# Kernel optimization log

Hardware: AMD Instinct MI355X
Metric: run time of the kernel (lower is better)

Reference implementation:

```python
import jax, jax.numpy as jnp
import numpy as np

N = 100000   # nodes
E = 3200000  # directed edges
IN = 128     # in_channels
H = 16       # hidden_channels
OUT = 2      # out_channels
EPS = 1e-5   # BatchNorm eps


def setup_inputs() -> dict:
    key = jax.random.key(0)
    ks = jax.random.split(key, 16)
    x = jax.random.normal(ks[0], (N, IN), jnp.float32)
    edge_index = jax.random.randint(ks[1], (2, E), 0, N, jnp.int32)

    def lin(k, fan_in, fan_out):
        return jax.random.normal(k, (fan_in, fan_out), jnp.float32) / np.sqrt(fan_in)

    return {
        "x": x,
        "edge_index": edge_index,
        "W1": lin(ks[2], IN, H), "b1": jnp.zeros((H,), jnp.float32),
        "W2": lin(ks[3], H, H), "b2": jnp.zeros((H,), jnp.float32),
        "W3": lin(ks[4], H, H), "b3": jnp.zeros((H,), jnp.float32),
        "gamma1": jnp.ones((H,), jnp.float32), "beta1": jnp.zeros((H,), jnp.float32),
        "gamma2": jnp.ones((H,), jnp.float32), "beta2": jnp.zeros((H,), jnp.float32),
        "Wfc": lin(ks[5], H, OUT), "bfc": jnp.zeros((OUT,), jnp.float32),
    }


def reference(x, edge_index, W1, b1, W2, b2, W3, b3,
              gamma1, beta1, gamma2, beta2, Wfc, bfc):
    src, dst = edge_index[0], edge_index[1]
    # symmetric GCN normalization with self loops: deg includes +1 self loop
    deg = jax.ops.segment_sum(jnp.ones((E,), x.dtype), dst, num_segments=N) + 1.0
    dis = jax.lax.rsqrt(deg)                      # [N]
    norm = dis[src] * dis[dst]                    # [E]

    def gcn_conv(h, W, b):
        hw = h @ W                                # [N, F] dense transform
        msg = norm[:, None] * hw[src]             # gather + scale  [E, F]
        agg = jax.ops.segment_sum(msg, dst, num_segments=N)
        agg = agg + (dis * dis)[:, None] * hw     # self-loop contribution
        return agg + b

    def batch_norm(h, g, be):
        mu = h.mean(axis=0)
        var = h.var(axis=0)
        return (h - mu) * jax.lax.rsqrt(var + EPS) * g + be

    h = batch_norm(jax.nn.relu(gcn_conv(x, W1, b1)), gamma1, beta1)
    # dropout is identity in inference / deterministic reference
    h = batch_norm(jax.nn.relu(gcn_conv(h, W2, b2)), gamma2, beta2)
    h = gcn_conv(h, W3, b3)
    return jax.nn.log_softmax(h @ Wfc + bfc, axis=1)
```

## Files before the change

### kernel.cpp

```cpp
#include <hip/hip_runtime.h>
#include <hip/hip_fp16.h>

#define NN 100000
#define EE 3200000
#define INC 128
#define HC 16
#define BN_EPS 1e-5f

#define NPB 256
#define NBUCK ((NN + NPB - 1) / NPB)
#define CAP 9216
#define BINSZ ((size_t)NBUCK * CAP)
#define BTILE 4096
#define BGRID ((EE + BTILE - 1) / BTILE)
#define SB_CAP 12288
#define GGRID 2048

#define XSTR 132

__device__ __forceinline__ __half2 bits_to_h2(int v) { __half2 h; *(int*)&h = v; return h; }
__device__ __forceinline__ int h2_to_bits(__half2 h) { return *(int*)&h; }


__global__ void init_cursor(int* __restrict__ bcursor) {
    int k = blockIdx.x * blockDim.x + threadIdx.x;
    if (k < NBUCK) bcursor[k] = k * CAP;
}


__global__ void bin_edges(const int* __restrict__ src, const int* __restrict__ dst,
                          int* __restrict__ bcursor, unsigned* __restrict__ bin) {
    __shared__ unsigned stage[BTILE];
    __shared__ unsigned short sbuck[BTILE];
    __shared__ int hist[NBUCK], loff[NBUCK], gbase[NBUCK];
    __shared__ int sc[512];
    int tid = threadIdx.x;
    for (int k = tid; k < NBUCK; k += 512) hist[k] = 0;
    __syncthreads();
    int e0 = blockIdx.x * BTILE;
    int cnt = min(BTILE, EE - e0);
    for (int i = tid; i < cnt; i += 512) atomicAdd(&hist[dst[e0 + i] >> 8], 1);
    __syncthreads();
    int hv = (tid < NBUCK) ? hist[tid] : 0;
    sc[tid] = hv;
    __syncthreads();
    for (int off = 1; off < 512; off <<= 1) {
        int t = (tid >= off) ? sc[tid - off] : 0;
        __syncthreads();
        sc[tid] += t;
        __syncthreads();
    }
    if (tid < NBUCK) {
        loff[tid] = sc[tid] - hv;
        if (hv) gbase[tid] = atomicAdd(&bcursor[tid], hv);
    }
    __syncthreads();
    for (int k = tid; k < NBUCK; k += 512) hist[k] = 0;
    __syncthreads();
    for (int i = tid; i < cnt; i += 512) {
        int d = dst[e0 + i], s = src[e0 + i];
        int k = d >> 8;
        int p = loff[k] + atomicAdd(&hist[k], 1);
        stage[p] = ((unsigned)(d & 255) << 24) | (unsigned)s;
        sbuck[p] = (unsigned short)k;
    }
    __syncthreads();
    for (int i = tid; i < cnt; i += 512) {
        int k = sbuck[i];
        int idx = gbase[k] + (i - loff[k]);
        if (idx < (k + 1) * CAP) bin[idx] = stage[i];
    }
}


__global__ __launch_bounds__(512) void sort_bucket(const int* __restrict__ bcursor,
                            const unsigned* __restrict__ bin,
                            unsigned* __restrict__ bin2, unsigned* __restrict__ rowpack,
                            float* __restrict__ dis) {
    __shared__ unsigned stg[SB_CAP];
    __shared__ int cnt[NPB], pos[NPB], sc[NPB];
    int tid = threadIdx.x;
    for (int k = tid; k < NPB; k += 512) cnt[k] = 0;
    __syncthreads();
    int b = blockIdx.x;
    int beg = b * CAP;
    int n = min(bcursor[b], beg + CAP) - beg;
    for (int i = tid; i < n; i += 512) {
        unsigned u = bin[beg + i];
        if (i < SB_CAP) stg[i] = u;
        atomicAdd(&cnt[u >> 24], 1);
    }
    __syncthreads();
    if (tid < NPB) sc[tid] = cnt[tid];
    __syncthreads();
    for (int off = 1; off < NPB; off <<= 1) {
        int t = 0;
        if (tid < NPB && tid >= off) t = sc[tid - off];
        __syncthreads();
        if (tid < NPB) sc[tid] += t;
        __syncthreads();
    }
    if (tid < NPB) {
        int v = cnt[tid];
        int lo = sc[tid] - v;
        pos[tid] = lo;
        int node = b * NPB + tid;
        if (node < NN) {
            rowpack[node] = ((unsigned)min(v, 1023) << 22) | (unsigned)(beg + lo);
            dis[node] = rsqrtf((float)v + 1.0f);
        }
    }
    __syncthreads();
    for (int i = tid; i < n; i += 512) {
        unsigned u = (i < SB_CAP) ? stg[i] : bin[beg + i];
        int nl = u >> 24;
        int p = atomicAdd(&pos[nl], 1);
        bin2[beg + p] = u & 0xFFFFFFu;
    }
}


__global__ void gemm_x_w1(const float* __restrict__ x, const float* __restrict__ W1,
                          const float* __restrict__ dis, __half2* __restrict__ hws2) {
    __shared__ float Ws[INC * HC];
    __shared__ float xs[16 * XSTR];
    int tid = threadIdx.x;
    for (int i = tid; i < INC * HC; i += 256) Ws[i] = W1[i];
    int node0 = blockIdx.x * 16;
    const float4* xsrc = (const float4*)(x + (size_t)node0 * INC);
    float4* xdst = (float4*)xs;
    int nvalid = min(16, NN - node0);
    int nf4 = nvalid * 32;
    for (int i = tid; i < nf4; i += 256) {
        int nl = i >> 5, k4 = i & 31;
        xdst[nl * 33 + k4] = xsrc[i];
    }
    __syncthreads();
    int c = tid & 15;
    int nl = tid >> 4;
    int node = node0 + nl;
    if (node >= NN) return;
    const float* xr = xs + nl * XSTR;
    float sum = 0.f;
#pragma unroll
    for (int k = 0; k < INC; ++k) sum += xr[k] * Ws[k * 16 + c];
    sum *= dis[node];
    float other = __shfl_xor(sum, 1);
    if ((c & 1) == 0) hws2[node * 8 + (c >> 1)] = __floats2half2_rn(sum, other);
}

__global__ void gemm_bn_h_w(const float* __restrict__ agg, const float* __restrict__ stats,
                            const float* __restrict__ gamma, const float* __restrict__ beta,
                            const float* __restrict__ W, const float* __restrict__ dis,
                            __half2* __restrict__ hws2) {
    __shared__ float Ws[HC * HC];
    __shared__ float sc[HC], sf[HC];
    int tid = threadIdx.x;
    if (tid < HC * HC) Ws[tid] = W[tid];
    if (tid < HC) {
        const float invN = 1.0f / NN;
        float mu = stats[tid] * invN;
        float var = stats[16 + tid] * invN - mu * mu;
        float rs = rsqrtf(var + BN_EPS);
        sc[tid] = gamma[tid] * rs;
        sf[tid] = beta[tid] - mu * gamma[tid] * rs;
    }
    __syncthreads();
    int i = blockIdx.x * 256 + tid;
    if (i >= NN * HC) return;
    int n = i >> 4, c = i & 15;
    const float4* ar = (const float4*)(agg + n * HC);
    float sum = 0.f;
#pragma unroll
    for (int q = 0; q < 4; ++q) {
        float4 v = ar[q];
        int k = q * 4;
        float h0 = fmaxf(v.x, 0.f) * sc[k + 0] + sf[k + 0];
        float h1 = fmaxf(v.y, 0.f) * sc[k + 1] + sf[k + 1];
        float h2 = fmaxf(v.z, 0.f) * sc[k + 2] + sf[k + 2];
        float h3 = fmaxf(v.w, 0.f) * sc[k + 3] + sf[k + 3];
        sum += h0 * Ws[(k + 0) * 16 + c] + h1 * Ws[(k + 1) * 16 + c]
             + h2 * Ws[(k + 2) * 16 + c] + h3 * Ws[(k + 3) * 16 + c];
    }
    sum *= dis[n];
    float other = __shfl_xor(sum, 1);
    if ((c & 1) == 0) hws2[n * 8 + (c >> 1)] = __floats2half2_rn(sum, other);
}


__global__ __launch_bounds__(256) void gcn_gather(const unsigned* __restrict__ rowpack,
                           const unsigned* __restrict__ bin2,
                           const float* __restrict__ dis, const __half2* __restrict__ hws2,
                           const float* __restrict__ b, float* __restrict__ agg,
                           float* __restrict__ stats) {
    __shared__ float acc[32];
    int tid = threadIdx.x;
    if (tid < 32) acc[tid] = 0.f;
    __syncthreads();
    int lane = tid & 63;
    int wid = tid >> 6;
    int cq = lane & 3;
    int slot = lane >> 2;
    const char* hbase = (const char*)hws2;
    float bc0 = b[4 * cq + 0], bc1 = b[4 * cq + 1], bc2 = b[4 * cq + 2], bc3 = b[4 * cq + 3];
    float s0 = 0.f, s1 = 0.f, s2 = 0.f, s3 = 0.f;
    float q0 = 0.f, q1 = 0.f, q2 = 0.f, q3 = 0.f;
    for (int node = blockIdx.x * 4 + wid; node < NN; node += GGRID * 4) {
        unsigned rp = rowpack[node];
        int beg = (int)(rp & 0x3FFFFFu);
        int end = beg + (int)(rp >> 22);
        int e0 = beg + slot;
        int i0 = (e0      < end) ? (int)bin2[e0]      : NN;
        int i1 = (e0 + 16 < end) ? (int)bin2[e0 + 16] : NN;
        int i2 = (e0 + 32 < end) ? (int)bin2[e0 + 32] : NN;
        int2 h0 = *(const int2*)(hbase + ((size_t)(unsigned)i0 << 5) + cq * 8);
        int2 h1 = *(const int2*)(hbase + ((size_t)(unsigned)i1 << 5) + cq * 8);
        int2 h2 = *(const int2*)(hbase + ((size_t)(unsigned)i2 << 5) + cq * 8);
        __half2 accA = __hadd2(__hadd2(bits_to_h2(h0.x), bits_to_h2(h1.x)), bits_to_h2(h2.x));
        __half2 accB = __hadd2(__hadd2(bits_to_h2(h0.y), bits_to_h2(h1.y)), bits_to_h2(h2.y));
        for (int e = e0 + 48; e < end; e += 16) {
            int s = (int)bin2[e];
            int2 hv = *(const int2*)(hbase + ((size_t)(unsigned)s << 5) + cq * 8);
            accA = __hadd2(accA, bits_to_h2(hv.x));
            accB = __hadd2(accB, bits_to_h2(hv.y));
        }
        int ia = h2_to_bits(accA), ib = h2_to_bits(accB);
#pragma unroll
        for (int d = 4; d < 64; d <<= 1) {
            int oa = __shfl_xor(ia, d), ob = __shfl_xor(ib, d);
            accA = __hadd2(accA, bits_to_h2(oa));
            accB = __hadd2(accB, bits_to_h2(ob));
            ia = h2_to_bits(accA); ib = h2_to_bits(accB);
        }
        if (slot == 0) {
            float d = dis[node];
            int2 ov = *(const int2*)(hbase + ((size_t)(unsigned)node << 5) + cq * 8);
            float2 sa = __half22float2(accA), sb = __half22float2(accB);
            float2 oa = __half22float2(bits_to_h2(ov.x)), ob = __half22float2(bits_to_h2(ov.y));
            float4 r;
            r.x = d * (sa.x + oa.x) + bc0;
            r.y = d * (sa.y + oa.y) + bc1;
            r.z = d * (sb.x + ob.x) + bc2;
            r.w = d * (sb.y + ob.y) + bc3;
            ((float4*)agg)[node * 4 + cq] = r;
            float t0 = fmaxf(r.x, 0.f), t1 = fmaxf(r.y, 0.f);
            float t2 = fmaxf(r.z, 0.f), t3 = fmaxf(r.w, 0.f);
            s0 += t0; s1 += t1; s2 += t2; s3 += t3;
            q0 += t0 * t0; q1 += t1 * t1; q2 += t2 * t2; q3 += t3 * t3;
        }
    }
    if (slot == 0) {
        atomicAdd(&acc[4 * cq + 0], s0);
        atomicAdd(&acc[4 * cq + 1], s1);
        atomicAdd(&acc[4 * cq + 2], s2);
        atomicAdd(&acc[4 * cq + 3], s3);
        atomicAdd(&acc[16 + 4 * cq + 0], q0);
        atomicAdd(&acc[16 + 4 * cq + 1], q1);
        atomicAdd(&acc[16 + 4 * cq + 2], q2);
        atomicAdd(&acc[16 + 4 * cq + 3], q3);
    }
    __syncthreads();
    if (tid < 32) atomicAdd(&stats[tid], acc[tid]);
}

__global__ __launch_bounds__(256) void gather_fc(const unsigned* __restrict__ rowpack,
                          const unsigned* __restrict__ bin2,
                          const float* __restrict__ dis, const __half2* __restrict__ hws2,
                          const float* __restrict__ b, const float* __restrict__ Wfc,
                          const float* __restrict__ bfc, float* __restrict__ out) {
    int tid = threadIdx.x;
    int lane = tid & 63;
    int wid = tid >> 6;
    int cq = lane & 3;
    int slot = lane >> 2;
    const char* hbase = (const char*)hws2;
    for (int node = blockIdx.x * 4 + wid; node < NN; node += GGRID * 4) {
        unsigned rp = rowpack[node];
        int beg = (int)(rp & 0x3FFFFFu);
        int end = beg + (int)(rp >> 22);
        int e0 = beg + slot;
        int i0 = (e0      < end) ? (int)bin2[e0]      : NN;
        int i1 = (e0 + 16 < end) ? (int)bin2[e0 + 16] : NN;
        int i2 = (e0 + 32 < end) ? (int)bin2[e0 + 32] : NN;
        int2 h0 = *(const int2*)(hbase + ((size_t)(unsigned)i0 << 5) + cq * 8);
        int2 h1 = *(const int2*)(hbase + ((size_t)(unsigned)i1 << 5) + cq * 8);
        int2 h2 = *(const int2*)(hbase + ((size_t)(unsigned)i2 << 5) + cq * 8);
        __half2 accA = __hadd2(__hadd2(bits_to_h2(h0.x), bits_to_h2(h1.x)), bits_to_h2(h2.x));
        __half2 accB = __hadd2(__hadd2(bits_to_h2(h0.y), bits_to_h2(h1.y)), bits_to_h2(h2.y));
        for (int e = e0 + 48; e < end; e += 16) {
            int s = (int)bin2[e];
            int2 hv = *(const int2*)(hbase + ((size_t)(unsigned)s << 5) + cq * 8);
            accA = __hadd2(accA, bits_to_h2(hv.x));
            accB = __hadd2(accB, bits_to_h2(hv.y));
        }
        int ia = h2_to_bits(accA), ib = h2_to_bits(accB);
#pragma unroll
        for (int d = 4; d < 64; d <<= 1) {
            int oa = __shfl_xor(ia, d), ob = __shfl_xor(ib, d);
            accA = __hadd2(accA, bits_to_h2(oa));
            accB = __hadd2(accB, bits_to_h2(ob));
            ia = h2_to_bits(accA); ib = h2_to_bits(accB);
        }
        float z0 = 0.f, z1 = 0.f;
        if (slot == 0) {
            float d = dis[node];
            int2 ov = *(const int2*)(hbase + ((size_t)(unsigned)node << 5) + cq * 8);
            float2 sa = __half22float2(accA), sb = __half22float2(accB);
            float2 oa = __half22float2(bits_to_h2(ov.x)), ob = __half22float2(bits_to_h2(ov.y));
            float v0 = d * (sa.x + oa.x) + b[4 * cq + 0];
            float v1 = d * (sa.y + oa.y) + b[4 * cq + 1];
            float v2 = d * (sb.x + ob.x) + b[4 * cq + 2];
            float v3 = d * (sb.y + ob.y) + b[4 * cq + 3];
            int k = 4 * cq;
            z0 = v0 * Wfc[(k + 0) * 2 + 0] + v1 * Wfc[(k + 1) * 2 + 0]
               + v2 * Wfc[(k + 2) * 2 + 0] + v3 * Wfc[(k + 3) * 2 + 0];
            z1 = v0 * Wfc[(k + 0) * 2 + 1] + v1 * Wfc[(k + 1) * 2 + 1]
               + v2 * Wfc[(k + 2) * 2 + 1] + v3 * Wfc[(k + 3) * 2 + 1];
        }
        z0 += __shfl_xor(z0, 1); z1 += __shfl_xor(z1, 1);
        z0 += __shfl_xor(z0, 2); z1 += __shfl_xor(z1, 2);
        if (lane == 0) {
            z0 += bfc[0]; z1 += bfc[1];
            float m = fmaxf(z0, z1);
            float lse = m + logf(expf(z0 - m) + expf(z1 - m));
            out[node * 2 + 0] = z0 - lse;
            out[node * 2 + 1] = z1 - lse;
        }
    }
}


extern "C" void kernel_launch(void* const* d_in, const int* in_sizes, int n_in,
                              void* d_out, int out_size, void* d_ws, size_t ws_size,
                              hipStream_t stream) {
    const float* x    = (const float*)d_in[0];
    const int*   ei   = (const int*)d_in[1];
    const int*   src  = ei;
    const int*   dstp = ei + EE;
    const float* W1   = (const float*)d_in[2];
    const float* b1   = (const float*)d_in[3];
    const float* W2   = (const float*)d_in[4];
    const float* b2   = (const float*)d_in[5];
    const float* W3   = (const float*)d_in[6];
    const float* b3   = (const float*)d_in[7];
    const float* g1   = (const float*)d_in[8];
    const float* be1  = (const float*)d_in[9];
    const float* g2   = (const float*)d_in[10];
    const float* be2  = (const float*)d_in[11];
    const float* Wfc  = (const float*)d_in[12];
    const float* bfc  = (const float*)d_in[13];
    float* out = (float*)d_out;

    char* p = (char*)d_ws;
    unsigned* bin   = (unsigned*)p;             p += BINSZ * 4;
    unsigned* bin2  = (unsigned*)p;             p += BINSZ * 4;
    __half2* hws2   = (__half2*)p;              p += (size_t)(NN + 1) * HC * 2;
    float*  agg     = (float*)p;                p += (size_t)NN * HC * 4;
    float*  dis     = (float*)p;                p += (size_t)NN * 4;
    unsigned* rowpack=(unsigned*)p;             p += (size_t)NN * 4;
    int*    bcursor = (int*)p;                  p += NBUCK * 4;
    float*  stats1  = (float*)p;                p += 32 * 4;
    float*  stats2  = (float*)p;                p += 32 * 4;

    const int TB = 256;
    const int gNH = (NN * HC + TB - 1) / TB;
    const int gX  = (NN + 15) / 16;

    init_cursor<<<2, 256, 0, stream>>>(bcursor);
    hipMemsetAsync(stats1, 0, 64 * sizeof(float), stream);
    hipMemsetAsync(hws2 + (size_t)NN * 8, 0, HC * 2, stream);
    bin_edges<<<BGRID, 512, 0, stream>>>(src, dstp, bcursor, bin);
    sort_bucket<<<NBUCK, 512, 0, stream>>>(bcursor, bin, bin2, rowpack, dis);

    gemm_x_w1<<<gX, TB, 0, stream>>>(x, W1, dis, hws2);
    gcn_gather<<<GGRID, TB, 0, stream>>>(rowpack, bin2, dis, hws2, b1, agg, stats1);

    gemm_bn_h_w<<<gNH, TB, 0, stream>>>(agg, stats1, g1, be1, W2, dis, hws2);
    gcn_gather<<<GGRID, TB, 0, stream>>>(rowpack, bin2, dis, hws2, b2, agg, stats2);

    gemm_bn_h_w<<<gNH, TB, 0, stream>>>(agg, stats2, g2, be2, W3, dis, hws2);
    gather_fc<<<GGRID, TB, 0, stream>>>(rowpack, bin2, dis, hws2, b3, Wfc, bfc, out);
}
```

Before: 267.7 us.

## Fold self-loop into CSR rows, use one wave per node, split BN stats

The bucket sort now places each node's own index as the first entry of its adjacency row, so the self-loop is gathered like any other edge and the separate self-feature load and dis lookup in the gather kernels go away. dis is recomputed from the stored row length. The gather kernels switch from a persistent grid-stride loop to one wave per node over a grid of N/4 blocks. BatchNorm statistics move out of the gather into a separate streaming reduction kernel over agg, which costs an extra pass over agg and an extra launch per layer.

```diff
diff --git a/kernel.cpp b/kernel.cpp
--- a/kernel.cpp
+++ b/kernel.cpp
@@ -14,7 +14,6 @@
 #define BTILE 4096
 #define BGRID ((EE + BTILE - 1) / BTILE)
 #define SB_CAP 12288
-#define GGRID 2048
 
 #define XSTR 132
 
@@ -91,7 +90,12 @@
         atomicAdd(&cnt[u >> 24], 1);
     }
     __syncthreads();
-    if (tid < NPB) sc[tid] = cnt[tid];
+    int node = b * NPB + tid;
+    int tot = 0;
+    if (tid < NPB) {
+        tot = cnt[tid] + ((node < NN) ? 1 : 0);
+        sc[tid] = tot;
+    }
     __syncthreads();
     for (int off = 1; off < NPB; off <<= 1) {
         int t = 0;
@@ -101,13 +105,14 @@
         __syncthreads();
     }
     if (tid < NPB) {
-        int v = cnt[tid];
-        int lo = sc[tid] - v;
-        pos[tid] = lo;
-        int node = b * NPB + tid;
+        int lo = sc[tid] - tot;
         if (node < NN) {
-            rowpack[node] = ((unsigned)min(v, 1023) << 22) | (unsigned)(beg + lo);
-            dis[node] = rsqrtf((float)v + 1.0f);
+            bin2[beg + lo] = (unsigned)node;
+            pos[tid] = lo + 1;
+            rowpack[node] = ((unsigned)min(tot, 1023) << 22) | (unsigned)(beg + lo);
+            dis[node] = rsqrtf((float)tot);
+        } else {
+            pos[tid] = lo;
         }
     }
     __syncthreads();
@@ -188,145 +193,147 @@
 }
 
 
-__global__ __launch_bounds__(256) void gcn_gather(const unsigned* __restrict__ rowpack,
+__global__ void gcn_gather(const unsigned* __restrict__ rowpack,
                            const unsigned* __restrict__ bin2,
-                           const float* __restrict__ dis, const __half2* __restrict__ hws2,
-                           const float* __restrict__ b, float* __restrict__ agg,
-                           float* __restrict__ stats) {
-    __shared__ float acc[32];
-    int tid = threadIdx.x;
-    if (tid < 32) acc[tid] = 0.f;
-    __syncthreads();
+                           const __half2* __restrict__ hws2,
+                           const float* __restrict__ b, float* __restrict__ agg) {
+    int tid = threadIdx.x;
     int lane = tid & 63;
-    int wid = tid >> 6;
+    int node = blockIdx.x * 4 + (tid >> 6);
+    if (node >= NN) return;
     int cq = lane & 3;
     int slot = lane >> 2;
+    unsigned rp = rowpack[node];
+    int beg = (int)(rp & 0x3FFFFFu);
+    int end = beg + (int)(rp >> 22);
     const char* hbase = (const char*)hws2;
-    float bc0 = b[4 * cq + 0], bc1 = b[4 * cq + 1], bc2 = b[4 * cq + 2], bc3 = b[4 * cq + 3];
+    int e0 = beg + slot;
+    int i0 = (e0      < end) ? (int)bin2[e0]      : NN;
+    int i1 = (e0 + 16 < end) ? (int)bin2[e0 + 16] : NN;
+    int i2 = (e0 + 32 < end) ? (int)bin2[e0 + 32] : NN;
+    int2 h0 = *(const int2*)(hbase + ((size_t)(unsigned)i0 << 5) + cq * 8);
+    int2 h1 = *(const int2*)(hbase + ((size_t)(unsigned)i1 << 5) + cq * 8);
+    int2 h2 = *(const int2*)(hbase + ((size_t)(unsigned)i2 << 5) + cq * 8);
+    __half2 accA = __hadd2(__hadd2(bits_to_h2(h0.x), bits_to_h2(h1.x)), bits_to_h2(h2.x));
+    __half2 accB = __hadd2(__hadd2(bits_to_h2(h0.y), bits_to_h2(h1.y)), bits_to_h2(h2.y));
+    for (int e = e0 + 48; e < end; e += 16) {
+        int s = (int)bin2[e];
+        int2 hv = *(const int2*)(hbase + ((size_t)(unsigned)s << 5) + cq * 8);
+        accA = __hadd2(accA, bits_to_h2(hv.x));
+        accB = __hadd2(accB, bits_to_h2(hv.y));
+    }
+    int ia = h2_to_bits(accA), ib = h2_to_bits(accB);
+#pragma unroll
+    for (int d = 4; d < 64; d <<= 1) {
+        int oa = __shfl_xor(ia, d), ob = __shfl_xor(ib, d);
+        accA = __hadd2(accA, bits_to_h2(oa));
+        accB = __hadd2(accB, bits_to_h2(ob));
+        ia = h2_to_bits(accA); ib = h2_to_bits(accB);
+    }
+    if (slot == 0) {
+        float d = rsqrtf((float)(rp >> 22));
+        float2 sa = __half22float2(accA), sb = __half22float2(accB);
+        float4 r;
+        r.x = d * sa.x + b[4 * cq + 0];
+        r.y = d * sa.y + b[4 * cq + 1];
+        r.z = d * sb.x + b[4 * cq + 2];
+        r.w = d * sb.y + b[4 * cq + 3];
+        ((float4*)agg)[node * 4 + cq] = r;
+    }
+}
+
+__global__ void gather_fc(const unsigned* __restrict__ rowpack,
+                          const unsigned* __restrict__ bin2,
+                          const __half2* __restrict__ hws2,
+                          const float* __restrict__ b, const float* __restrict__ Wfc,
+                          const float* __restrict__ bfc, float* __restrict__ out) {
+    int tid = threadIdx.x;
+    int lane = tid & 63;
+    int node = blockIdx.x * 4 + (tid >> 6);
+    if (node >= NN) return;
+    int cq = lane & 3;
+    int slot = lane >> 2;
+    unsigned rp = rowpack[node];
+    int beg = (int)(rp & 0x3FFFFFu);
+    int end = beg + (int)(rp >> 22);
+    const char* hbase = (const char*)hws2;
+    int e0 = beg + slot;
+    int i0 = (e0      < end) ? (int)bin2[e0]      : NN;
+    int i1 = (e0 + 16 < end) ? (int)bin2[e0 + 16] : NN;
+    int i2 = (e0 + 32 < end) ? (int)bin2[e0 + 32] : NN;
+    int2 h0 = *(const int2*)(hbase + ((size_t)(unsigned)i0 << 5) + cq * 8);
+    int2 h1 = *(const int2*)(hbase + ((size_t)(unsigned)i1 << 5) + cq * 8);
+    int2 h2 = *(const int2*)(hbase + ((size_t)(unsigned)i2 << 5) + cq * 8);
+    __half2 accA = __hadd2(__hadd2(bits_to_h2(h0.x), bits_to_h2(h1.x)), bits_to_h2(h2.x));
+    __half2 accB = __hadd2(__hadd2(bits_to_h2(h0.y), bits_to_h2(h1.y)), bits_to_h2(h2.y));
+    for (int e = e0 + 48; e < end; e += 16) {
+        int s = (int)bin2[e];
+        int2 hv = *(const int2*)(hbase + ((size_t)(unsigned)s << 5) + cq * 8);
+        accA = __hadd2(accA, bits_to_h2(hv.x));
+        accB = __hadd2(accB, bits_to_h2(hv.y));
+    }
+    int ia = h2_to_bits(accA), ib = h2_to_bits(accB);
+#pragma unroll
+    for (int d = 4; d < 64; d <<= 1) {
+        int oa = __shfl_xor(ia, d), ob = __shfl_xor(ib, d);
+        accA = __hadd2(accA, bits_to_h2(oa));
+        accB = __hadd2(accB, bits_to_h2(ob));
+        ia = h2_to_bits(accA); ib = h2_to_bits(accB);
+    }
+    float z0 = 0.f, z1 = 0.f;
+    if (slot == 0) {
+        float d = rsqrtf((float)(rp >> 22));
+        float2 sa = __half22float2(accA), sb = __half22float2(accB);
+        float v0 = d * sa.x + b[4 * cq + 0];
+        float v1 = d * sa.y + b[4 * cq + 1];
+        float v2 = d * sb.x + b[4 * cq + 2];
+        float v3 = d * sb.y + b[4 * cq + 3];
+        int k = 4 * cq;
+        z0 = v0 * Wfc[(k + 0) * 2 + 0] + v1 * Wfc[(k + 1) * 2 + 0]
+           + v2 * Wfc[(k + 2) * 2 + 0] + v3 * Wfc[(k + 3) * 2 + 0];
+        z1 = v0 * Wfc[(k + 0) * 2 + 1] + v1 * Wfc[(k + 1) * 2 + 1]
+           + v2 * Wfc[(k + 2) * 2 + 1] + v3 * Wfc[(k + 3) * 2 + 1];
+    }
+    z0 += __shfl_xor(z0, 1); z1 += __shfl_xor(z1, 1);
+    z0 += __shfl_xor(z0, 2); z1 += __shfl_xor(z1, 2);
+    if (lane == 0) {
+        z0 += bfc[0]; z1 += bfc[1];
+        float m = fmaxf(z0, z1);
+        float lse = m + logf(expf(z0 - m) + expf(z1 - m));
+        out[node * 2 + 0] = z0 - lse;
+        out[node * 2 + 1] = z1 - lse;
+    }
+}
+
+
+__global__ void bn_stats_final(const float* __restrict__ agg, float* __restrict__ stats) {
+    int tid = threadIdx.x;
     float s0 = 0.f, s1 = 0.f, s2 = 0.f, s3 = 0.f;
     float q0 = 0.f, q1 = 0.f, q2 = 0.f, q3 = 0.f;
-    for (int node = blockIdx.x * 4 + wid; node < NN; node += GGRID * 4) {
-        unsigned rp = rowpack[node];
-        int beg = (int)(rp & 0x3FFFFFu);
-        int end = beg + (int)(rp >> 22);
-        int e0 = beg + slot;
-        int i0 = (e0      < end) ? (int)bin2[e0]      : NN;
-        int i1 = (e0 + 16 < end) ? (int)bin2[e0 + 16] : NN;
-        int i2 = (e0 + 32 < end) ? (int)bin2[e0 + 32] : NN;
-        int2 h0 = *(const int2*)(hbase + ((size_t)(unsigned)i0 << 5) + cq * 8);
-        int2 h1 = *(const int2*)(hbase + ((size_t)(unsigned)i1 << 5) + cq * 8);
-        int2 h2 = *(const int2*)(hbase + ((size_t)(unsigned)i2 << 5) + cq * 8);
-        __half2 accA = __hadd2(__hadd2(bits_to_h2(h0.x), bits_to_h2(h1.x)), bits_to_h2(h2.x));
-        __half2 accB = __hadd2(__hadd2(bits_to_h2(h0.y), bits_to_h2(h1.y)), bits_to_h2(h2.y));
-        for (int e = e0 + 48; e < end; e += 16) {
-            int s = (int)bin2[e];
-            int2 hv = *(const int2*)(hbase + ((size_t)(unsigned)s << 5) + cq * 8);
-            accA = __hadd2(accA, bits_to_h2(hv.x));
-            accB = __hadd2(accB, bits_to_h2(hv.y));
-        }
-        int ia = h2_to_bits(accA), ib = h2_to_bits(accB);
-#pragma unroll
-        for (int d = 4; d < 64; d <<= 1) {
-            int oa = __shfl_xor(ia, d), ob = __shfl_xor(ib, d);
-            accA = __hadd2(accA, bits_to_h2(oa));
-            accB = __hadd2(accB, bits_to_h2(ob));
-            ia = h2_to_bits(accA); ib = h2_to_bits(accB);
-        }
-        if (slot == 0) {
-            float d = dis[node];
-            int2 ov = *(const int2*)(hbase + ((size_t)(unsigned)node << 5) + cq * 8);
-            float2 sa = __half22float2(accA), sb = __half22float2(accB);
-            float2 oa = __half22float2(bits_to_h2(ov.x)), ob = __half22float2(bits_to_h2(ov.y));
-            float4 r;
-            r.x = d * (sa.x + oa.x) + bc0;
-            r.y = d * (sa.y + oa.y) + bc1;
-            r.z = d * (sb.x + ob.x) + bc2;
-            r.w = d * (sb.y + ob.y) + bc3;
-            ((float4*)agg)[node * 4 + cq] = r;
-            float t0 = fmaxf(r.x, 0.f), t1 = fmaxf(r.y, 0.f);
-            float t2 = fmaxf(r.z, 0.f), t3 = fmaxf(r.w, 0.f);
-            s0 += t0; s1 += t1; s2 += t2; s3 += t3;
-            q0 += t0 * t0; q1 += t1 * t1; q2 += t2 * t2; q3 += t3 * t3;
-        }
-    }
-    if (slot == 0) {
-        atomicAdd(&acc[4 * cq + 0], s0);
-        atomicAdd(&acc[4 * cq + 1], s1);
-        atomicAdd(&acc[4 * cq + 2], s2);
-        atomicAdd(&acc[4 * cq + 3], s3);
-        atomicAdd(&acc[16 + 4 * cq + 0], q0);
-        atomicAdd(&acc[16 + 4 * cq + 1], q1);
-        atomicAdd(&acc[16 + 4 * cq + 2], q2);
-        atomicAdd(&acc[16 + 4 * cq + 3], q3);
-    }
+    const float4* a4 = (const float4*)agg;
+    const int n4 = NN * HC / 4;
+    int i0 = blockIdx.x * 256 + tid;
+    for (int i = i0; i < n4; i += gridDim.x * 256) {
+        float4 v = a4[i];
+        float r0 = fmaxf(v.x, 0.f), r1 = fmaxf(v.y, 0.f);
+        float r2 = fmaxf(v.z, 0.f), r3 = fmaxf(v.w, 0.f);
+        s0 += r0; s1 += r1; s2 += r2; s3 += r3;
+        q0 += r0 * r0; q1 += r1 * r1; q2 += r2 * r2; q3 += r3 * r3;
+    }
+    int quad = i0 & 3;
+    __shared__ float acc[32];
+    if (tid < 32) acc[tid] = 0.f;
+    __syncthreads();
+    atomicAdd(&acc[4 * quad + 0], s0);
+    atomicAdd(&acc[4 * quad + 1], s1);
+    atomicAdd(&acc[4 * quad + 2], s2);
+    atomicAdd(&acc[4 * quad + 3], s3);
+    atomicAdd(&acc[16 + 4 * quad + 0], q0);
+    atomicAdd(&acc[16 + 4 * quad + 1], q1);
+    atomicAdd(&acc[16 + 4 * quad + 2], q2);
+    atomicAdd(&acc[16 + 4 * quad + 3], q3);
     __syncthreads();
     if (tid < 32) atomicAdd(&stats[tid], acc[tid]);
-}
-
-__global__ __launch_bounds__(256) void gather_fc(const unsigned* __restrict__ rowpack,
-                          const unsigned* __restrict__ bin2,
-                          const float* __restrict__ dis, const __half2* __restrict__ hws2,
-                          const float* __restrict__ b, const float* __restrict__ Wfc,
-                          const float* __restrict__ bfc, float* __restrict__ out) {
-    int tid = threadIdx.x;
-    int lane = tid & 63;
-    int wid = tid >> 6;
-    int cq = lane & 3;
-    int slot = lane >> 2;
-    const char* hbase = (const char*)hws2;
-    for (int node = blockIdx.x * 4 + wid; node < NN; node += GGRID * 4) {
-        unsigned rp = rowpack[node];
-        int beg = (int)(rp & 0x3FFFFFu);
-        int end = beg + (int)(rp >> 22);
-        int e0 = beg + slot;
-        int i0 = (e0      < end) ? (int)bin2[e0]      : NN;
-        int i1 = (e0 + 16 < end) ? (int)bin2[e0 + 16] : NN;
-        int i2 = (e0 + 32 < end) ? (int)bin2[e0 + 32] : NN;
-        int2 h0 = *(const int2*)(hbase + ((size_t)(unsigned)i0 << 5) + cq * 8);
-        int2 h1 = *(const int2*)(hbase + ((size_t)(unsigned)i1 << 5) + cq * 8);
-        int2 h2 = *(const int2*)(hbase + ((size_t)(unsigned)i2 << 5) + cq * 8);
-        __half2 accA = __hadd2(__hadd2(bits_to_h2(h0.x), bits_to_h2(h1.x)), bits_to_h2(h2.x));
-        __half2 accB = __hadd2(__hadd2(bits_to_h2(h0.y), bits_to_h2(h1.y)), bits_to_h2(h2.y));
-        for (int e = e0 + 48; e < end; e += 16) {
-            int s = (int)bin2[e];
-            int2 hv = *(const int2*)(hbase + ((size_t)(unsigned)s << 5) + cq * 8);
-            accA = __hadd2(accA, bits_to_h2(hv.x));
-            accB = __hadd2(accB, bits_to_h2(hv.y));
-        }
-        int ia = h2_to_bits(accA), ib = h2_to_bits(accB);
-#pragma unroll
-        for (int d = 4; d < 64; d <<= 1) {
-            int oa = __shfl_xor(ia, d), ob = __shfl_xor(ib, d);
-            accA = __hadd2(accA, bits_to_h2(oa));
-            accB = __hadd2(accB, bits_to_h2(ob));
-            ia = h2_to_bits(accA); ib = h2_to_bits(accB);
-        }
-        float z0 = 0.f, z1 = 0.f;
-        if (slot == 0) {
-            float d = dis[node];
-            int2 ov = *(const int2*)(hbase + ((size_t)(unsigned)node << 5) + cq * 8);
-            float2 sa = __half22float2(accA), sb = __half22float2(accB);
-            float2 oa = __half22float2(bits_to_h2(ov.x)), ob = __half22float2(bits_to_h2(ov.y));
-            float v0 = d * (sa.x + oa.x) + b[4 * cq + 0];
-            float v1 = d * (sa.y + oa.y) + b[4 * cq + 1];
-            float v2 = d * (sb.x + ob.x) + b[4 * cq + 2];
-            float v3 = d * (sb.y + ob.y) + b[4 * cq + 3];
-            int k = 4 * cq;
-            z0 = v0 * Wfc[(k + 0) * 2 + 0] + v1 * Wfc[(k + 1) * 2 + 0]
-               + v2 * Wfc[(k + 2) * 2 + 0] + v3 * Wfc[(k + 3) * 2 + 0];
-            z1 = v0 * Wfc[(k + 0) * 2 + 1] + v1 * Wfc[(k + 1) * 2 + 1]
-               + v2 * Wfc[(k + 2) * 2 + 1] + v3 * Wfc[(k + 3) * 2 + 1];
-        }
-        z0 += __shfl_xor(z0, 1); z1 += __shfl_xor(z1, 1);
-        z0 += __shfl_xor(z0, 2); z1 += __shfl_xor(z1, 2);
-        if (lane == 0) {
-            z0 += bfc[0]; z1 += bfc[1];
-            float m = fmaxf(z0, z1);
-            float lse = m + logf(expf(z0 - m) + expf(z1 - m));
-            out[node * 2 + 0] = z0 - lse;
-            out[node * 2 + 1] = z1 - lse;
-        }
-    }
 }
 
 
@@ -365,6 +372,7 @@
     const int TB = 256;
     const int gNH = (NN * HC + TB - 1) / TB;
     const int gX  = (NN + 15) / 16;
+    const int gG  = (NN + 3) / 4;
 
     init_cursor<<<2, 256, 0, stream>>>(bcursor);
     hipMemsetAsync(stats1, 0, 64 * sizeof(float), stream);
@@ -373,11 +381,13 @@
     sort_bucket<<<NBUCK, 512, 0, stream>>>(bcursor, bin, bin2, rowpack, dis);
 
     gemm_x_w1<<<gX, TB, 0, stream>>>(x, W1, dis, hws2);
-    gcn_gather<<<GGRID, TB, 0, stream>>>(rowpack, bin2, dis, hws2, b1, agg, stats1);
+    gcn_gather<<<gG, TB, 0, stream>>>(rowpack, bin2, hws2, b1, agg);
+    bn_stats_final<<<1024, TB, 0, stream>>>(agg, stats1);
 
     gemm_bn_h_w<<<gNH, TB, 0, stream>>>(agg, stats1, g1, be1, W2, dis, hws2);
-    gcn_gather<<<GGRID, TB, 0, stream>>>(rowpack, bin2, dis, hws2, b2, agg, stats2);
+    gcn_gather<<<gG, TB, 0, stream>>>(rowpack, bin2, hws2, b2, agg);
+    bn_stats_final<<<1024, TB, 0, stream>>>(agg, stats2);
 
     gemm_bn_h_w<<<gNH, TB, 0, stream>>>(agg, stats2, g2, be2, W3, dis, hws2);
-    gather_fc<<<GGRID, TB, 0, stream>>>(rowpack, bin2, dis, hws2, b3, Wfc, bfc, out);
-}
+    gather_fc<<<gG, TB, 0, stream>>>(rowpack, bin2, hws2, b3, Wfc, bfc, out);
+}
```

Measured after the change: 266.8 us. About the same (-0.3%).
